# Optimization experiments

Hardware: AMD Instinct MI355X
Metric: run time of the kernel (lower is better)

Reference implementation:

```python
import jax, jax.numpy as jnp
import numpy as np

N = 100000  # nodes
K = 6       # kNN neighbors (includes self, loop=True)


def _knn_edges(pos_np, k):
    """Exact kNN with self-loops, chunked to bound memory. Returns (src, dst) int32."""
    n = pos_np.shape[0]
    idx = np.empty((n, k), dtype=np.int32)
    sq = (pos_np ** 2).sum(1)
    cs = 512
    for s in range(0, n, cs):
        e = min(s + cs, n)
        d = sq[s:e, None] - 2.0 * (pos_np[s:e] @ pos_np.T) + sq[None, :]
        idx[s:e] = np.argpartition(d, k, axis=1)[:, :k].astype(np.int32)
    src = idx.reshape(-1)                                  # neighbors j
    dst = np.repeat(np.arange(n, dtype=np.int32), k)       # centers i
    return src, dst


def _linear_init(key, fan_in, fan_out):
    k1, k2 = jax.random.split(key)
    s = 1.0 / np.sqrt(fan_in)
    W = jax.random.uniform(k1, (fan_in, fan_out), minval=-s, maxval=s, dtype=jnp.float32)
    b = jax.random.uniform(k2, (fan_out,), minval=-s, maxval=s, dtype=jnp.float32)
    return W, b


def setup_inputs() -> dict:
    rng = np.random.default_rng(0)
    pos_np = rng.standard_normal((N, 3)).astype(np.float32)
    src, dst = _knn_edges(pos_np, K)
    edge_index = jnp.asarray(np.stack([src, dst]))

    key = jax.random.key(0)
    ks = jax.random.split(key, 6)
    W1a, b1a = _linear_init(ks[0], 3 + 3, 32)
    W1b, b1b = _linear_init(ks[1], 32, 32)
    W2a, b2a = _linear_init(ks[2], 32 + 3, 64)
    W2b, b2b = _linear_init(ks[3], 64, 64)
    W3a, b3a = _linear_init(ks[4], 64 + 3, 128)
    W3b, b3b = _linear_init(ks[5], 128, 128)

    return dict(pos=jnp.asarray(pos_np), edge_index=edge_index,
                W1a=W1a, b1a=b1a, W1b=W1b, b1b=b1b,
                W2a=W2a, b2a=b2a, W2b=W2b, b2b=b2b,
                W3a=W3a, b3a=b3a, W3b=W3b, b3b=b3b)


def _pointnet_conv(x, pos, src, dst, Wa, ba, Wb, bb):
    # message per edge (j->i): local_nn(concat(x_j, pos_j - pos_i)); max-aggregate at i
    m = jnp.concatenate([x[src], pos[src] - pos[dst]], axis=-1)  # [E, Cin+3]
    m = jax.nn.relu(m @ Wa + ba) @ Wb + bb                       # [E, Cout]
    return jax.ops.segment_max(m, dst, num_segments=N)           # [N, Cout]


def reference(pos, edge_index, W1a, b1a, W1b, b1b, W2a, b2a, W2b, b2b, W3a, b3a, W3b, b3b):
    src, dst = edge_index[0], edge_index[1]
    h = jax.nn.relu(_pointnet_conv(pos, pos, src, dst, W1a, b1a, W1b, b1b))
    h = jax.nn.relu(_pointnet_conv(h, pos, src, dst, W2a, b2a, W2b, b2b))
    h = jax.nn.relu(_pointnet_conv(h, pos, src, dst, W3a, b3a, W3b, b3b))
    return h
```

## Files before the change

### kernel.cpp

```cpp
#include <hip/hip_runtime.h>

#define NODES 100000
#define KNN 6

typedef unsigned short u16t;
typedef __attribute__((ext_vector_type(8))) short bf16x8;
typedef __attribute__((ext_vector_type(4))) float f32x4;
union U16 { uint4 u; bf16x8 b; };

__device__ inline f32x4 mfma16(bf16x8 a, bf16x8 b, f32x4 c) {
    return __builtin_amdgcn_mfma_f32_16x16x32_bf16(a, b, c, 0, 0, 0);
}
__device__ inline unsigned top2(unsigned u1, unsigned u0) {
    return __builtin_amdgcn_perm(u1, u0, 0x07060302u);
}
__device__ inline u16t bf16_rn(float x) {
    unsigned u = __float_as_uint(x);
    return (u16t)((u + 0x7FFF + ((u >> 16) & 1)) >> 16);
}
__device__ inline float bf16_f(u16t h) {
    return __uint_as_float(((unsigned)h) << 16);
}
__device__ inline void split_store(u16t* hp, u16t* lp, float v) {
    const unsigned u = __float_as_uint(v);
    *hp = (u16t)(u >> 16);
    const float hif = __uint_as_float(u & 0xFFFF0000u);
    *lp = (u16t)(__float_as_uint(v - hif) >> 16);
}

template <int CIN_, int N_>
__device__ void prep_dev(const float* __restrict__ W,
                         uint4* __restrict__ fh, uint4* __restrict__ fl, int idx) {
    constexpr int KT = (CIN_ + 31) / 32;
    constexpr int NTt = N_ / 16;
    if (idx >= NTt * KT * 64) return;
    const int lane = idx & 63;
    const int fk = idx >> 6;
    const int kt = fk % KT, t = fk / KT;
    const int n = t * 16 + (lane & 15);
    const int kbase = kt * 32 + (lane >> 4) * 8;
    unsigned h[4], l[4];
    for (int p = 0; p < 4; p++) {
        u16t hh[2], ll[2];
        for (int q = 0; q < 2; q++) {
            const int c = kbase + 2 * p + q;
            const float w = (c < CIN_) ? W[(size_t)c * N_ + n] : 0.f;
            const u16t hi = bf16_rn(w);
            hh[q] = hi;
            ll[q] = bf16_rn(w - bf16_f(hi));
        }
        h[p] = (unsigned)hh[0] | ((unsigned)hh[1] << 16);
        l[p] = (unsigned)ll[0] | ((unsigned)ll[1] << 16);
    }
    fh[idx] = make_uint4(h[0], h[1], h[2], h[3]);
    fl[idx] = make_uint4(l[0], l[1], l[2], l[3]);
}

__global__ void prep_all(const float* W1a, const float* W1b,
                         const float* W2a, const float* W2b,
                         const float* W3a, const float* W3b, uint4* wf) {
    const int b = blockIdx.x, t = threadIdx.x;
    if (b == 0)      prep_dev<6, 32>(W1a, wf + 0, wf + 128, t);
    else if (b == 1) prep_dev<32, 32>(W1b, wf + 256, wf + 384, t);
    else if (b < 4)  prep_dev<35, 64>(W2a, wf + 512, wf + 1024, (b - 2) * 256 + t);
    else if (b < 6)  prep_dev<64, 64>(W2b, wf + 1536, wf + 2048, (b - 4) * 256 + t);
    else if (b < 12) prep_dev<67, 128>(W3a, wf + 2560, wf + 4096, (b - 6) * 256 + t);
    else             prep_dev<128, 128>(W3b, wf + 5632, wf + 7680, (b - 12) * 256 + t);
}

template <int CX, int H, int NWAVE, int NB, bool OUTP>
__global__ __launch_bounds__(NWAVE * 64, 4) void pnconv_mfma(
    const u16t* __restrict__ xh, const u16t* __restrict__ xl,
    const float* __restrict__ pos, const int* __restrict__ ei,
    const uint4* __restrict__ wfa_hi, const uint4* __restrict__ wfa_lo,
    const float* __restrict__ ba,
    const uint4* __restrict__ wfb_hi, const uint4* __restrict__ wfb_lo,
    const float* __restrict__ bb,
    float* __restrict__ outf, u16t* __restrict__ oh, u16t* __restrict__ ol)
{
    constexpr int NTH = NWAVE * 64;
    constexpr int CIN = CX + 3;
    constexpr int K1T = (CIN + 31) / 32;
    constexpr int K2T = H / 32;
    constexpr int NW = (H / 16) / NWAVE;
    constexpr int E = NB * KNN;
    constexpr int MT1 = E / 16;
    constexpr int MT2 = E / 16;
    constexpr int K1P = K1T * 32 + 8;
    constexpr int K2P = K2T * 32 + 8;
    constexpr int APL = E * K1P;
    constexpr int HPL = E * K2P;
    constexpr int SM = (2 * APL > 2 * HPL) ? 2 * APL : 2 * HPL;
    static_assert(E % 48 == 0 && E <= NTH, "tile shape");
    static_assert(MT2 % 3 == 0, "slot perm needs m-triples");

    __shared__ __align__(16) u16t smem[SM];
    __shared__ int srcs[E];

    const int tid = threadIdx.x;
    const int lane = tid & 63, wv = tid >> 6;
    const int l15 = lane & 15, quad = lane >> 4;
    const int node0 = blockIdx.x * NB;
    const long e0 = (long)node0 * KNN;

    if (tid < E) srcs[tid] = ei[e0 + tid];

    U16 wah[2][NW], wal[2][NW];
#pragma unroll
    for (int t = 0; t < NW; t++) {
        const int fi = ((wv * NW + t) * K1T) * 64 + lane;
        wah[0][t].u = wfa_hi[fi];
        wal[0][t].u = wfa_lo[fi];
    }
    __syncthreads();

    if constexpr (CX % 8 == 0) {
        constexpr int C8 = CX / 8;
        for (int i = tid; i < E * C8; i += NTH) {
            const int e = i / C8, c0 = i % C8;
            const int c = (c0 + e) & (C8 - 1);
            const size_t sb = (size_t)srcs[e] * CX + c * 8;
            *(uint4*)&smem[e * K1P + c * 8] = *(const uint4*)&xh[sb];
            *(uint4*)&smem[APL + e * K1P + c * 8] = *(const uint4*)&xl[sb];
        }
    }
    for (int i = tid; i < E * 3; i += NTH) {
        const int e = i / 3, d = i - 3 * (i / 3);
        const int s = srcs[e], nd = node0 + e / KNN;
        const float sp = pos[3 * s + d];
        if constexpr (CX == 3)
            split_store(&smem[e * K1P + d], &smem[APL + e * K1P + d], sp);
        split_store(&smem[e * K1P + CX + d], &smem[APL + e * K1P + CX + d],
                    sp - pos[3 * nd + d]);
    }
    constexpr int PADA = (CIN + 7) & ~7;
    constexpr int NU4 = (K1P - PADA) / 8;
    for (int i = tid; i < 2 * E; i += NTH) {
        const int pl = (i >= E) ? 1 : 0;
        const int e = i - pl * E;
        u16t* row = &smem[pl * APL + e * K1P];
        for (int k = CIN; k < PADA; k++) row[k] = 0;
        for (int j = 0; j < NU4; j++) *(uint4*)&row[PADA + j * 8] = make_uint4(0, 0, 0, 0);
    }
    __syncthreads();

    f32x4 acc1[NW][MT1];
#pragma unroll
    for (int t = 0; t < NW; t++)
#pragma unroll
        for (int m = 0; m < MT1; m++) acc1[t][m] = (f32x4){0.f, 0.f, 0.f, 0.f};

#pragma unroll
    for (int kt = 0; kt < K1T; kt++) {
        const int cur = kt & 1, nxt = cur ^ 1;
        const int nkt = (kt + 1 < K1T) ? kt + 1 : kt;
#pragma unroll
        for (int t = 0; t < NW; t++) {
            const int fi = ((wv * NW + t) * K1T + nkt) * 64 + lane;
            wah[nxt][t].u = wfa_hi[fi];
            wal[nxt][t].u = wfa_lo[fi];
        }
#pragma unroll
        for (int m = 0; m < MT1; m++) {
            const u16t* p = &smem[(m * 16 + l15) * K1P + kt * 32 + quad * 8];
            U16 dh, dl;
            dh.u = *(const uint4*)p;
            dl.u = *(const uint4*)(p + APL);
#pragma unroll
            for (int t = 0; t < NW; t++) {
                acc1[t][m] = mfma16(wah[cur][t].b, dh.b, acc1[t][m]);
                acc1[t][m] = mfma16(wah[cur][t].b, dl.b, acc1[t][m]);
                acc1[t][m] = mfma16(wal[cur][t].b, dh.b, acc1[t][m]);
            }
        }
    }

    U16 wbh[2][NW], wbl[2][NW];
#pragma unroll
    for (int t = 0; t < NW; t++) {
        const int fi = ((wv * NW + t) * K2T) * 64 + lane;
        wbh[0][t].u = wfb_hi[fi];
        wbl[0][t].u = wfb_lo[fi];
    }
    __syncthreads();

#pragma unroll
    for (int t = 0; t < NW; t++) {
        const int khb = (wv * NW + t) * 16 + quad * 4;
        const float4 bs = *(const float4*)&ba[khb];
#pragma unroll
        for (int m = 0; m < MT1; m++) {
            const float v0 = fmaxf(acc1[t][m][0] + bs.x, 0.f);
            const float v1 = fmaxf(acc1[t][m][1] + bs.y, 0.f);
            const float v2 = fmaxf(acc1[t][m][2] + bs.z, 0.f);
            const float v3 = fmaxf(acc1[t][m][3] + bs.w, 0.f);
            const unsigned u0 = __float_as_uint(v0), u1 = __float_as_uint(v1);
            const unsigned u2 = __float_as_uint(v2), u3 = __float_as_uint(v3);
            uint2 hw, lw;
            hw.x = top2(u1, u0);
            hw.y = top2(u3, u2);
            const float l0 = v0 - __uint_as_float(u0 & 0xFFFF0000u);
            const float l1 = v1 - __uint_as_float(u1 & 0xFFFF0000u);
            const float l2 = v2 - __uint_as_float(u2 & 0xFFFF0000u);
            const float l3 = v3 - __uint_as_float(u3 & 0xFFFF0000u);
            lw.x = top2(__float_as_uint(l1), __float_as_uint(l0));
            lw.y = top2(__float_as_uint(l3), __float_as_uint(l2));
            u16t* wp = &smem[(m * 16 + l15) * K2P + khb];
            *(uint2*)wp = hw;
            *(uint2*)(wp + HPL) = lw;
        }
    }
    __syncthreads();

    int eaddr[MT2];
#pragma unroll
    for (int m = 0; m < MT2; m++) {
        const int nd_s = (m / 3) * 8 + 2 * (l15 >> 2) + ((l15 >> 1) & 1);
        const int i_s = (m % 3) * 2 + (l15 & 1);
        eaddr[m] = (nd_s * KNN + i_s) * K2P + quad * 8;
    }

    f32x4 acc2[NW][MT2];
#pragma unroll
    for (int t = 0; t < NW; t++)
#pragma unroll
        for (int m = 0; m < MT2; m++) acc2[t][m] = (f32x4){0.f, 0.f, 0.f, 0.f};

#pragma unroll
    for (int kt = 0; kt < K2T; kt++) {
        const int cur = kt & 1, nxt = cur ^ 1;
        const int nkt = (kt + 1 < K2T) ? kt + 1 : kt;
#pragma unroll
        for (int t = 0; t < NW; t++) {
            const int fi = ((wv * NW + t) * K2T + nkt) * 64 + lane;
            wbh[nxt][t].u = wfb_hi[fi];
            wbl[nxt][t].u = wfb_lo[fi];
        }
#pragma unroll
        for (int m = 0; m < MT2; m++) {
            const u16t* p = &smem[eaddr[m] + kt * 32];
            U16 dh, dl;
            dh.u = *(const uint4*)p;
            dl.u = *(const uint4*)(p + HPL);
#pragma unroll
            for (int t = 0; t < NW; t++) {
                acc2[t][m] = mfma16(dh.b, wbh[cur][t].b, acc2[t][m]);
                acc2[t][m] = mfma16(dh.b, wbl[cur][t].b, acc2[t][m]);
                acc2[t][m] = mfma16(dl.b, wbh[cur][t].b, acc2[t][m]);
            }
        }
    }

#pragma unroll
    for (int t = 0; t < NW; t++) {
        const int nb = (wv * NW + t) * 16;
        const float bias = bb[nb + l15];
#pragma unroll
        for (int g = 0; g < MT2 / 3; g++) {
#pragma unroll
            for (int rp = 0; rp < 2; rp++) {
                float v = fmaxf(
                    fmaxf(fmaxf(acc2[t][3 * g + 0][2 * rp], acc2[t][3 * g + 0][2 * rp + 1]),
                          fmaxf(acc2[t][3 * g + 1][2 * rp], acc2[t][3 * g + 1][2 * rp + 1])),
                    fmaxf(acc2[t][3 * g + 2][2 * rp], acc2[t][3 * g + 2][2 * rp + 1]));
                v = fmaxf(v + bias, 0.f);
                const int node = node0 + g * 8 + 2 * quad + rp;
                const size_t oidx = (size_t)node * H + nb + l15;
                if constexpr (OUTP) {
                    split_store(&oh[oidx], &ol[oidx], v);
                } else {
                    outf[oidx] = v;
                }
            }
        }
    }
}

extern "C" void kernel_launch(void* const* d_in, const int* in_sizes, int n_in,
                              void* d_out, int out_size, void* d_ws, size_t ws_size,
                              hipStream_t stream) {
    const float* pos = (const float*)d_in[0];
    const int* ei = (const int*)d_in[1];
    const float* W1a = (const float*)d_in[2];
    const float* b1a = (const float*)d_in[3];
    const float* W1b = (const float*)d_in[4];
    const float* b1b = (const float*)d_in[5];
    const float* W2a = (const float*)d_in[6];
    const float* b2a = (const float*)d_in[7];
    const float* W2b = (const float*)d_in[8];
    const float* b2b = (const float*)d_in[9];
    const float* W3a = (const float*)d_in[10];
    const float* b3a = (const float*)d_in[11];
    const float* W3b = (const float*)d_in[12];
    const float* b3b = (const float*)d_in[13];

    u16t* h1h = (u16t*)d_ws;
    u16t* h1l = h1h + (size_t)NODES * 32;
    u16t* h2h = h1l + (size_t)NODES * 32;
    u16t* h2l = h2h + (size_t)NODES * 64;
    uint4* wf = (uint4*)(h2l + (size_t)NODES * 64);

    prep_all<<<20, 256, 0, stream>>>(W1a, W1b, W2a, W2b, W3a, W3b, wf);

    pnconv_mfma<3, 32, 2, 16, true><<<NODES / 16, 128, 0, stream>>>(
        nullptr, nullptr, pos, ei,
        wf + 0, wf + 128, b1a, wf + 256, wf + 384, b1b,
        nullptr, h1h, h1l);

    pnconv_mfma<32, 64, 4, 16, true><<<NODES / 16, 256, 0, stream>>>(
        h1h, h1l, pos, ei,
        wf + 512, wf + 1024, b2a, wf + 1536, wf + 2048, b2b,
        nullptr, h2h, h2l);

    pnconv_mfma<64, 128, 4, 8, false><<<NODES / 8, 256, 0, stream>>>(
        h2h, h2l, pos, ei,
        wf + 2560, wf + 4096, b3a, wf + 5632, wf + 7680, b3b,
        (float*)d_out, nullptr, nullptr);
}
```

Before: 235.2 us.

## Fold relative-position term into fp32 FMA epilogue, shrink first GEMM K

For layers 2 and 3, the three relative-position input channels are removed from the MFMA GEMM. The first-layer K dimension drops from 35/67 to 32/64, which removes a whole 32-wide K tile along with its split-bf16 triple MFMAs and the zero-padding pass. The dpos contribution is now added in fp32 with scalar FMAs using weights read directly from the original W matrices, and the dpos values are staged in shared memory. The redundant last-iteration weight prefetch is also skipped. The cost is some extra VALU work and a few more registers per thread.

```diff
diff --git a/kernel.cpp b/kernel.cpp
--- a/kernel.cpp
+++ b/kernel.cpp
@@ -62,10 +62,10 @@
     const int b = blockIdx.x, t = threadIdx.x;
     if (b == 0)      prep_dev<6, 32>(W1a, wf + 0, wf + 128, t);
     else if (b == 1) prep_dev<32, 32>(W1b, wf + 256, wf + 384, t);
-    else if (b < 4)  prep_dev<35, 64>(W2a, wf + 512, wf + 1024, (b - 2) * 256 + t);
-    else if (b < 6)  prep_dev<64, 64>(W2b, wf + 1536, wf + 2048, (b - 4) * 256 + t);
-    else if (b < 12) prep_dev<67, 128>(W3a, wf + 2560, wf + 4096, (b - 6) * 256 + t);
-    else             prep_dev<128, 128>(W3b, wf + 5632, wf + 7680, (b - 12) * 256 + t);
+    else if (b == 2) prep_dev<32, 64>(W2a, wf + 512, wf + 768, t);
+    else if (b < 5)  prep_dev<64, 64>(W2b, wf + 1024, wf + 1536, (b - 3) * 256 + t);
+    else if (b < 9)  prep_dev<64, 128>(W3a, wf + 2048, wf + 3072, (b - 5) * 256 + t);
+    else             prep_dev<128, 128>(W3b, wf + 4096, wf + 6144, (b - 9) * 256 + t);
 }
 
 template <int CX, int H, int NWAVE, int NB, bool OUTP>
@@ -76,10 +76,12 @@
     const float* __restrict__ ba,
     const uint4* __restrict__ wfb_hi, const uint4* __restrict__ wfb_lo,
     const float* __restrict__ bb,
+    const float* __restrict__ wpos,
     float* __restrict__ outf, u16t* __restrict__ oh, u16t* __restrict__ ol)
 {
     constexpr int NTH = NWAVE * 64;
-    constexpr int CIN = CX + 3;
+    constexpr bool PK = (CX == 3);
+    constexpr int CIN = PK ? CX + 3 : CX;
     constexpr int K1T = (CIN + 31) / 32;
     constexpr int K2T = H / 32;
     constexpr int NW = (H / 16) / NWAVE;
@@ -93,9 +95,11 @@
     constexpr int SM = (2 * APL > 2 * HPL) ? 2 * APL : 2 * HPL;
     static_assert(E % 48 == 0 && E <= NTH, "tile shape");
     static_assert(MT2 % 3 == 0, "slot perm needs m-triples");
+    static_assert(PK || (2 * APL + E * 8) <= SM, "dpos overlay fits");
 
     __shared__ __align__(16) u16t smem[SM];
     __shared__ int srcs[E];
+    float* const dpf = (float*)&smem[2 * APL];
 
     const int tid = threadIdx.x;
     const int lane = tid & 63, wv = tid >> 6;
@@ -111,6 +115,15 @@
         const int fi = ((wv * NW + t) * K1T) * 64 + lane;
         wah[0][t].u = wfa_hi[fi];
         wal[0][t].u = wfa_lo[fi];
+    }
+    f32x4 wpp[NW][3];
+    if constexpr (!PK) {
+#pragma unroll
+        for (int t = 0; t < NW; t++)
+#pragma unroll
+            for (int d = 0; d < 3; d++)
+                wpp[t][d] = *(const f32x4*)&wpos[(size_t)(CX + d) * H +
+                                                (wv * NW + t) * 16 + quad * 4];
     }
     __syncthreads();
 
@@ -128,19 +141,24 @@
         const int e = i / 3, d = i - 3 * (i / 3);
         const int s = srcs[e], nd = node0 + e / KNN;
         const float sp = pos[3 * s + d];
-        if constexpr (CX == 3)
+        const float dl = sp - pos[3 * nd + d];
+        if constexpr (PK) {
             split_store(&smem[e * K1P + d], &smem[APL + e * K1P + d], sp);
-        split_store(&smem[e * K1P + CX + d], &smem[APL + e * K1P + CX + d],
-                    sp - pos[3 * nd + d]);
-    }
-    constexpr int PADA = (CIN + 7) & ~7;
-    constexpr int NU4 = (K1P - PADA) / 8;
-    for (int i = tid; i < 2 * E; i += NTH) {
-        const int pl = (i >= E) ? 1 : 0;
-        const int e = i - pl * E;
-        u16t* row = &smem[pl * APL + e * K1P];
-        for (int k = CIN; k < PADA; k++) row[k] = 0;
-        for (int j = 0; j < NU4; j++) *(uint4*)&row[PADA + j * 8] = make_uint4(0, 0, 0, 0);
+            split_store(&smem[e * K1P + CX + d], &smem[APL + e * K1P + CX + d], dl);
+        } else {
+            dpf[e * 4 + d] = dl;
+        }
+    }
+    if constexpr (PK) {
+        constexpr int PADA = (CIN + 7) & ~7;
+        constexpr int NU4 = (K1P - PADA) / 8;
+        for (int i = tid; i < 2 * E; i += NTH) {
+            const int pl = (i >= E) ? 1 : 0;
+            const int e = i - pl * E;
+            u16t* row = &smem[pl * APL + e * K1P];
+            for (int k = CIN; k < PADA; k++) row[k] = 0;
+            for (int j = 0; j < NU4; j++) *(uint4*)&row[PADA + j * 8] = make_uint4(0, 0, 0, 0);
+        }
     }
     __syncthreads();
 
@@ -153,12 +171,13 @@
 #pragma unroll
     for (int kt = 0; kt < K1T; kt++) {
         const int cur = kt & 1, nxt = cur ^ 1;
-        const int nkt = (kt + 1 < K1T) ? kt + 1 : kt;
-#pragma unroll
-        for (int t = 0; t < NW; t++) {
-            const int fi = ((wv * NW + t) * K1T + nkt) * 64 + lane;
-            wah[nxt][t].u = wfa_hi[fi];
-            wal[nxt][t].u = wfa_lo[fi];
+        if (kt + 1 < K1T) {
+#pragma unroll
+            for (int t = 0; t < NW; t++) {
+                const int fi = ((wv * NW + t) * K1T + kt + 1) * 64 + lane;
+                wah[nxt][t].u = wfa_hi[fi];
+                wal[nxt][t].u = wfa_lo[fi];
+            }
         }
 #pragma unroll
         for (int m = 0; m < MT1; m++) {
@@ -181,6 +200,19 @@
         const int fi = ((wv * NW + t) * K2T) * 64 + lane;
         wbh[0][t].u = wfb_hi[fi];
         wbl[0][t].u = wfb_lo[fi];
+    }
+
+    if constexpr (!PK) {
+#pragma unroll
+        for (int m = 0; m < MT1; m++) {
+            const f32x4 dp = *(const f32x4*)&dpf[(m * 16 + l15) * 4];
+#pragma unroll
+            for (int t = 0; t < NW; t++)
+#pragma unroll
+                for (int j = 0; j < 4; j++)
+                    acc1[t][m][j] += wpp[t][0][j] * dp[0] + wpp[t][1][j] * dp[1]
+                                   + wpp[t][2][j] * dp[2];
+        }
     }
     __syncthreads();
 
@@ -229,12 +261,13 @@
 #pragma unroll
     for (int kt = 0; kt < K2T; kt++) {
         const int cur = kt & 1, nxt = cur ^ 1;
-        const int nkt = (kt + 1 < K2T) ? kt + 1 : kt;
-#pragma unroll
-        for (int t = 0; t < NW; t++) {
-            const int fi = ((wv * NW + t) * K2T + nkt) * 64 + lane;
-            wbh[nxt][t].u = wfb_hi[fi];
-            wbl[nxt][t].u = wfb_lo[fi];
+        if (kt + 1 < K2T) {
+#pragma unroll
+            for (int t = 0; t < NW; t++) {
+                const int fi = ((wv * NW + t) * K2T + kt + 1) * 64 + lane;
+                wbh[nxt][t].u = wfb_hi[fi];
+                wbl[nxt][t].u = wfb_lo[fi];
+            }
         }
 #pragma unroll
         for (int m = 0; m < MT2; m++) {
@@ -300,20 +333,20 @@
     u16t* h2l = h2h + (size_t)NODES * 64;
     uint4* wf = (uint4*)(h2l + (size_t)NODES * 64);
 
-    prep_all<<<20, 256, 0, stream>>>(W1a, W1b, W2a, W2b, W3a, W3b, wf);
+    prep_all<<<17, 256, 0, stream>>>(W1a, W1b, W2a, W2b, W3a, W3b, wf);
 
     pnconv_mfma<3, 32, 2, 16, true><<<NODES / 16, 128, 0, stream>>>(
         nullptr, nullptr, pos, ei,
         wf + 0, wf + 128, b1a, wf + 256, wf + 384, b1b,
-        nullptr, h1h, h1l);
+        nullptr, nullptr, h1h, h1l);
 
     pnconv_mfma<32, 64, 4, 16, true><<<NODES / 16, 256, 0, stream>>>(
         h1h, h1l, pos, ei,
-        wf + 512, wf + 1024, b2a, wf + 1536, wf + 2048, b2b,
-        nullptr, h2h, h2l);
+        wf + 512, wf + 768, b2a, wf + 1024, wf + 1536, b2b,
+        W2a, nullptr, h2h, h2l);
 
     pnconv_mfma<64, 128, 4, 8, false><<<NODES / 8, 256, 0, stream>>>(
         h2h, h2l, pos, ei,
-        wf + 2560, wf + 4096, b3a, wf + 5632, wf + 7680, b3b,
-        (float*)d_out, nullptr, nullptr);
-}
+        wf + 2048, wf + 3072, b3a, wf + 4096, wf + 6144, b3b,
+        W3a, (float*)d_out, nullptr, nullptr);
+}
```

Result: no change. 230.8 us (-1.9%).
